# Optimization experiments

Hardware: AMD Instinct MI355X
Metric: run time of the kernel (lower is better)

Reference implementation:

```python
import jax, jax.numpy as jnp
import numpy as np
import math

B, S, HID, H = 2, 2048, 2048, 16
D = HID // H  # head_dim = 128


def rotate_half(x):
    x1, x2 = x[..., : x.shape[-1] // 2], x[..., x.shape[-1] // 2:]
    return jnp.concatenate((-x2, x1), axis=-1)


def setup_inputs() -> dict:
    key = jax.random.key(0)
    ks = jax.random.split(key, 6)
    x = jax.random.normal(ks[0], (B, S, HID), dtype=jnp.float32)
    # learned projection weights (torch Linear: y = x @ W.T); store as [in, out]
    scale = 1.0 / math.sqrt(HID)
    Wq = jax.random.normal(ks[1], (HID, HID), dtype=jnp.float32) * scale
    Wk = jax.random.normal(ks[2], (HID, HID), dtype=jnp.float32) * scale
    Wv = jax.random.normal(ks[3], (HID, HID), dtype=jnp.float32) * scale
    Wo = jax.random.normal(ks[4], (HID, HID), dtype=jnp.float32) * scale
    # causal additive mask [1,1,S,S]
    causal = jnp.tril(jnp.ones((S, S), dtype=bool))
    attention_mask = jnp.where(causal, 0.0, -1e9).astype(jnp.float32)[None, None]
    # ALiBi bias: slope per head times key position, broadcast over queries
    slopes = 2.0 ** (-8.0 * (jnp.arange(1, H + 1, dtype=jnp.float32) / H))
    alibi = (-slopes[:, None] * jnp.arange(S, dtype=jnp.float32)[None, :])[None, :, None, :]  # [1,H,1,S]
    # RoPE tables broadcastable to [B,H,S,D]
    inv_freq = 1.0 / (10000.0 ** (jnp.arange(0, D // 2, dtype=jnp.float32) / (D // 2)))
    t = jnp.arange(S, dtype=jnp.float32)
    freqs = t[:, None] * inv_freq[None, :]            # [S, D/2]
    emb = jnp.concatenate((freqs, freqs), axis=-1)    # [S, D]
    freqs_cos = jnp.cos(emb)[None, None]              # [1,1,S,D]
    freqs_sin = jnp.sin(emb)[None, None]
    return {"x": x, "Wq": Wq, "Wk": Wk, "Wv": Wv, "Wo": Wo,
            "attention_mask": attention_mask, "alibi": alibi,
            "freqs_cos": freqs_cos, "freqs_sin": freqs_sin}


def reference(x, Wq, Wk, Wv, Wo, attention_mask, alibi, freqs_cos, freqs_sin):
    b, s, _ = x.shape
    def split_heads(y):
        return y.reshape(b, s, H, D).transpose(0, 2, 1, 3)  # [B,H,S,D]
    q = split_heads(x @ Wq)
    k = split_heads(x @ Wk)
    v = split_heads(x @ Wv)
    q = q * freqs_cos + rotate_half(q) * freqs_sin
    k = k * freqs_cos + rotate_half(k) * freqs_sin
    scores = jnp.einsum('bhqd,bhkd->bhqk', q, k) / math.sqrt(D)
    scores = scores + attention_mask + alibi
    attn = jax.nn.softmax(scores, axis=-1)  # dropout p=0 (eval) -> identity
    out = jnp.einsum('bhqk,bhkd->bhqd', attn, v)
    out = out.transpose(0, 2, 1, 3).reshape(b, s, HID)
    return out @ Wo
```

## Files before the change

### kernel.cpp

```cpp
#include <hip/hip_runtime.h>

#define S_LEN   2048
#define HEADS   16
#define HID_DIM 2048
#define HEAD_D  128
#define BATCH   2

typedef __bf16          bf16x8 __attribute__((ext_vector_type(8)));
typedef unsigned short  u16x8  __attribute__((ext_vector_type(8)));
typedef unsigned short  u16x4  __attribute__((ext_vector_type(4)));
typedef float           f32x4  __attribute__((ext_vector_type(4)));

__device__ __forceinline__ unsigned short f2bf(float f) {
  unsigned u = __builtin_bit_cast(unsigned, f);
  u += 0x7FFFu + ((u >> 16) & 1u);
  return (unsigned short)(u >> 16);
}
__device__ __forceinline__ float bf2f(unsigned short s) {
  unsigned u = ((unsigned)s) << 16;
  return __builtin_bit_cast(float, u);
}

__device__ __forceinline__ f32x4 mfma16(u16x8 a, u16x8 b, f32x4 c) {
  return __builtin_amdgcn_mfma_f32_16x16x32_bf16(
      __builtin_bit_cast(bf16x8, a), __builtin_bit_cast(bf16x8, b), c, 0, 0, 0);
}

__device__ __forceinline__ void async_load16(const void* g, void* l) {
  __builtin_amdgcn_global_load_lds(
      (const __attribute__((address_space(1))) void*)g,
      (__attribute__((address_space(3))) void*)l, 16, 0, 0);
}

__global__ __launch_bounds__(256) void cvt_bf16(const float* __restrict__ in,
                                                unsigned short* __restrict__ out,
                                                int n8) {
  for (int i = blockIdx.x * blockDim.x + threadIdx.x; i < n8;
       i += gridDim.x * blockDim.x) {
    const float4* p = (const float4*)in + 2L * i;
    float4 a = p[0], b = p[1];
    u16x8 v;
    v[0] = f2bf(a.x); v[1] = f2bf(a.y); v[2] = f2bf(a.z); v[3] = f2bf(a.w);
    v[4] = f2bf(b.x); v[5] = f2bf(b.y); v[6] = f2bf(b.z); v[7] = f2bf(b.w);
    ((u16x8*)out)[i] = v;
  }
}

__global__ __launch_bounds__(256) void transpose_cvt3(
    const float* __restrict__ W0, const float* __restrict__ W1,
    const float* __restrict__ W2, unsigned short* __restrict__ O0,
    unsigned short* __restrict__ O1, unsigned short* __restrict__ O2,
    int dim) {
  __shared__ float tile[32][33];
  const int z = blockIdx.z;
  const float* W = (z == 0) ? W0 : (z == 1) ? W1 : W2;
  unsigned short* Wt = (z == 0) ? O0 : (z == 1) ? O1 : O2;
  const int bx = blockIdx.x * 32, by = blockIdx.y * 32;
  const int tx = threadIdx.x, ty = threadIdx.y;
#pragma unroll
  for (int i = 0; i < 32; i += 8)
    tile[ty + i][tx] = W[(long)(by + ty + i) * dim + bx + tx];
  __syncthreads();
#pragma unroll
  for (int i = 0; i < 32; i += 8)
    Wt[(long)(bx + ty + i) * dim + by + tx] = f2bf(tile[tx][ty + i]);
}

__global__ __launch_bounds__(256) void transpose_cvt(const float* __restrict__ W,
                                                     unsigned short* __restrict__ Wt,
                                                     int dim) {
  __shared__ float tile[32][33];
  const int bx = blockIdx.x * 32, by = blockIdx.y * 32;
  const int tx = threadIdx.x, ty = threadIdx.y;
#pragma unroll
  for (int i = 0; i < 32; i += 8)
    tile[ty + i][tx] = W[(long)(by + ty + i) * dim + bx + tx];
  __syncthreads();
#pragma unroll
  for (int i = 0; i < 32; i += 8)
    Wt[(long)(bx + ty + i) * dim + by + tx] = f2bf(tile[tx][ty + i]);
}

__global__ __launch_bounds__(256) void transpose_v(const unsigned short* __restrict__ V,
                                                   unsigned short* __restrict__ Vt) {
  __shared__ unsigned short tile[32][34];
  const int s0 = blockIdx.x * 32, d0 = blockIdx.y * 32, bh = blockIdx.z;
  const int b = bh >> 4, h = bh & 15;
  const int tx = threadIdx.x, ty = threadIdx.y;
#pragma unroll
  for (int i = 0; i < 32; i += 8)
    tile[ty + i][tx] =
        V[(long)(b * S_LEN + s0 + ty + i) * HID_DIM + h * HEAD_D + d0 + tx];
  __syncthreads();
#pragma unroll
  for (int i = 0; i < 32; i += 8)
    Vt[((long)bh * HEAD_D + d0 + ty + i) * S_LEN + s0 + tx] = tile[tx][ty + i];
}

__global__ __launch_bounds__(256) void rope_qk(unsigned short* __restrict__ Qb,
                                               unsigned short* __restrict__ Kb,
                                               const float* __restrict__ fcos,
                                               const float* __restrict__ fsin) {
  const float SC = 0.08838834764831845f;
  const long i = (long)blockIdx.x * blockDim.x + threadIdx.x;
  const int d = (int)(i & 63);
  const int h = (int)((i >> 6) & (HEADS - 1));
  const long row = i >> 10;
  const int s = (int)(row & (S_LEN - 1));
  const long base = row * HID_DIM + h * HEAD_D + d;
  const float c0 = fcos[s * HEAD_D + d], c1 = fcos[s * HEAD_D + d + 64];
  const float s0 = fsin[s * HEAD_D + d], s1 = fsin[s * HEAD_D + d + 64];
  const float q0 = bf2f(Qb[base]), q1 = bf2f(Qb[base + 64]);
  Qb[base]      = f2bf((q0 * c0 - q1 * s0) * SC);
  Qb[base + 64] = f2bf((q1 * c1 + q0 * s1) * SC);
  const float k0 = bf2f(Kb[base]), k1 = bf2f(Kb[base + 64]);
  Kb[base]      = f2bf(k0 * c0 - k1 * s0);
  Kb[base + 64] = f2bf(k1 * c1 + k0 * s1);
}

__global__ __launch_bounds__(256, 3) void gemm10(
    const unsigned short* __restrict__ A,
    const unsigned short* __restrict__ Bt0,
    unsigned short* __restrict__ Cb0,
    float* __restrict__ Cf,
    int M, int N, int K, long zsB, long zsC) {
  __shared__ __align__(16) unsigned short Abuf[3][128 * 32];
  __shared__ __align__(16) unsigned short Bbuf[3][128 * 32];
  const int t = threadIdx.x;
  const int lane = t & 63;
  const int w = t >> 6;
  const int wr = w >> 1, wc = w & 1;
  const int l15 = lane & 15, l4 = lane >> 4;

  const int nwg = gridDim.x;
  const int bid = blockIdx.x;
  const int sw = (bid & 7) * (nwg >> 3) + (bid >> 3);
  const int nbx = N >> 7, nby = M >> 7;
  const int z = sw / (nbx * nby);
  const int rem = sw - z * nbx * nby;
  const int by = rem / nbx;
  const int bx = rem - by * nbx;

  const unsigned short* Bt = Bt0 + (long)z * zsB;
  unsigned short* Cb = Cb0 ? Cb0 + (long)z * zsC : nullptr;

  f32x4 acc[4][4] = {};

  const int kcol = 8 * ((t & 3) ^ ((t >> 3) & 3));
  const unsigned short* aSrc = A + ((long)by * 128 + (t >> 2)) * K + kcol;
  const unsigned short* bSrc = Bt + ((long)bx * 128 + (t >> 2)) * K + kcol;

  const int swzr = 8 * (l4 ^ ((l15 >> 1) & 3));
  const int aROff = (wr * 64 + l15) * 32 + swzr;
  const int bROff = (wc * 64 + l15) * 32 + swzr;

  const int NT = K >> 5;

#define STG(slot, kt_) do {                                              \
    async_load16(aSrc + (long)(kt_) * 32,                                \
                 (char*)(&Abuf[slot][0]) + t * 16);                      \
    async_load16(aSrc + (long)(kt_) * 32 + 64L * K,                      \
                 (char*)(&Abuf[slot][0]) + 4096 + t * 16);               \
    async_load16(bSrc + (long)(kt_) * 32,                                \
                 (char*)(&Bbuf[slot][0]) + t * 16);                      \
    async_load16(bSrc + (long)(kt_) * 32 + 64L * K,                      \
                 (char*)(&Bbuf[slot][0]) + 4096 + t * 16);               \
  } while (0)

  STG(0, 0);
  STG(1, 1);
  asm volatile("s_waitcnt vmcnt(4)" ::: "memory");
  __builtin_amdgcn_s_barrier();

  int cur = 0;
  for (int kt = 0; kt < NT; ++kt) {
    const unsigned short* Ab = &Abuf[cur][0];
    const unsigned short* Bb = &Bbuf[cur][0];
    const bool stg = (kt + 2) < NT;
    u16x8 af[4], bfr[4];
#pragma unroll
    for (int n = 0; n < 4; ++n) bfr[n] = *(const u16x8*)&Bb[bROff + n * 512];
#pragma unroll
    for (int m = 0; m < 4; ++m) af[m] = *(const u16x8*)&Ab[aROff + m * 512];
    if (stg) {
      const int s2 = (cur + 2 >= 3) ? cur - 1 : cur + 2;
      STG(s2, kt + 2);
    }
    __builtin_amdgcn_s_setprio(1);
#pragma unroll
    for (int m = 0; m < 4; ++m)
#pragma unroll
      for (int n = 0; n < 4; ++n)
        acc[m][n] = mfma16(af[m], bfr[n], acc[m][n]);
    __builtin_amdgcn_s_setprio(0);
    __builtin_amdgcn_sched_barrier(0);
    if (kt + 1 < NT) {
      if (stg) asm volatile("s_waitcnt vmcnt(4)" ::: "memory");
      else     asm volatile("s_waitcnt vmcnt(0)" ::: "memory");
      __builtin_amdgcn_s_barrier();
    }
    cur = (cur + 1 >= 3) ? 0 : cur + 1;
  }
#undef STG

  const long orow = (long)by * 128 + wr * 64 + l4 * 4;
  const long ocol = (long)bx * 128 + wc * 64 + l15;
#pragma unroll
  for (int m = 0; m < 4; ++m)
#pragma unroll
    for (int n = 0; n < 4; ++n)
#pragma unroll
      for (int r = 0; r < 4; ++r) {
        const long row = orow + m * 16 + r;
        const long col = ocol + n * 16;
        if (Cb) Cb[row * N + col] = f2bf(acc[m][n][r]);
        else    Cf[row * N + col] = acc[m][n][r];
      }
}

__global__ __launch_bounds__(256, 4) void attn_fwd7(
    const unsigned short* __restrict__ Q,
    const unsigned short* __restrict__ K,
    const unsigned short* __restrict__ Vt,
    const float* __restrict__ alibi,
    unsigned short* __restrict__ O) {
  __shared__ __align__(16) unsigned short Kl[2][32 * 128];
  __shared__ __align__(16) unsigned short Vl[2][64 * 64];
  __shared__ __align__(16) unsigned short Pl[4][32][40];
  const int t = threadIdx.x;
  const int lane = t & 63;
  const int w = t >> 6;
  const int l15 = lane & 15, l4 = lane >> 4;

  const int bid = blockIdx.x;
  const int xcd = bid & 7;
  const int idx = bid >> 3;
  const int qh = idx >> 4;
  const int ql = idx & 15;
  const int qt = (qh < 2) ? ql : (15 - ql);
  const int bh = xcd * 4 + qh;
  const int b = bh >> 4, h = bh & 15;
  const int q0b = qt * 128;
  const int q0 = q0b + w * 32;
  const float nslope = alibi[h * S_LEN + 1];

  const long rowbase = ((long)b * S_LEN) * HID_DIM + h * HEAD_D;
  const long vtbase  = ((long)bh * HEAD_D) * S_LEN;

  u16x8 qf[2][4];
  {
    const unsigned short* qp = Q + rowbase + (long)(q0 + l15) * HID_DIM + l4 * 8;
#pragma unroll
    for (int m = 0; m < 2; ++m)
#pragma unroll
      for (int ds = 0; ds < 4; ++ds)
        qf[m][ds] = *(const u16x8*)(qp + (long)m * 16 * HID_DIM + ds * 32);
  }

  f32x4 acc[2][8] = {};
  float m_r[2] = {-1e30f, -1e30f};
  float l_r[2] = {0.f, 0.f};

  int dd, rw, cbl;
  dd = 16 * t;        rw = dd >> 8; cbl = (dd & 255) ^ ((rw & 7) << 4);
  const unsigned short* ksrc0 = K + rowbase + (long)rw * HID_DIM + (cbl >> 1);
  dd = 4096 + 16 * t; rw = dd >> 8; cbl = (dd & 255) ^ ((rw & 7) << 4);
  const unsigned short* ksrc1 = K + rowbase + (long)rw * HID_DIM + (cbl >> 1);
  dd = 16 * t;        rw = dd >> 7; cbl = (dd & 127) ^ ((rw & 3) << 4);
  const unsigned short* vsrc0 =
      Vt + vtbase + (long)(2 * rw + (cbl >> 6)) * S_LEN + ((cbl & 63) >> 1);
  dd = 4096 + 16 * t; rw = dd >> 7; cbl = (dd & 127) ^ ((rw & 3) << 4);
  const unsigned short* vsrc1 =
      Vt + vtbase + (long)(2 * rw + (cbl >> 6)) * S_LEN + ((cbl & 63) >> 1);

#define ASTAGE(buf, kt_) do {                                             \
    const long kadd = (long)(kt_) * 32 * HID_DIM;                         \
    async_load16(ksrc0 + kadd, (char*)(&Kl[buf][0]) + 16 * t);            \
    async_load16(ksrc1 + kadd, (char*)(&Kl[buf][0]) + 4096 + 16 * t);     \
    async_load16(vsrc0 + (kt_) * 32, (char*)(&Vl[buf][0]) + 16 * t);      \
    async_load16(vsrc1 + (kt_) * 32, (char*)(&Vl[buf][0]) + 4096 + 16 * t); \
  } while (0)

  const int ntB = qt * 4 + 4;
  const int mykt = q0 >> 5;

  ASTAGE(0, 0);
  __syncthreads();

  int cur = 0;
  for (int kt = 0; kt < ntB; ++kt) {
    const int kb = kt * 32;
    if (kt + 1 < ntB) ASTAGE(cur ^ 1, kt + 1);
    if (kt <= mykt) {
      const char* Kc = (const char*)&Kl[cur][0];
      const char* Vc = (const char*)&Vl[cur][0];
      f32x4 sacc[2][2] = {};
#pragma unroll
      for (int ds = 0; ds < 4; ++ds) {
        u16x8 kfr[2];
#pragma unroll
        for (int n = 0; n < 2; ++n) {
          const int R = 16 * n + l15;
          const int cb = (ds * 64 + l4 * 16) ^ ((l15 & 7) << 4);
          kfr[n] = *(const u16x8*)(Kc + R * 256 + cb);
        }
#pragma unroll
        for (int n = 0; n < 2; ++n)
#pragma unroll
          for (int m = 0; m < 2; ++m)
            sacc[n][m] = mfma16(kfr[n], qf[m][ds], sacc[n][m]);
      }
#pragma unroll
      for (int m = 0; m < 2; ++m) {
        const int q = q0 + 16 * m + l15;
        float pv[2][4];
        float rmax = -1e30f;
#pragma unroll
        for (int n = 0; n < 2; ++n)
#pragma unroll
          for (int r = 0; r < 4; ++r) {
            const int k = kb + 16 * n + l4 * 4 + r;
            float v = sacc[n][m][r] + nslope * (float)k;
            if (k > q) v = -1e30f;
            pv[n][r] = v;
            rmax = fmaxf(rmax, v);
          }
        rmax = fmaxf(rmax, __shfl_xor(rmax, 16, 64));
        rmax = fmaxf(rmax, __shfl_xor(rmax, 32, 64));
        const float mnew = fmaxf(m_r[m], rmax);
        const float sf = __expf(m_r[m] - mnew);
        m_r[m] = mnew;
        float rsum = 0.f;
#pragma unroll
        for (int n = 0; n < 2; ++n)
#pragma unroll
          for (int r = 0; r < 4; ++r) {
            pv[n][r] = __expf(pv[n][r] - mnew);
            rsum += pv[n][r];
          }
        rsum += __shfl_xor(rsum, 16, 64);
        rsum += __shfl_xor(rsum, 32, 64);
        l_r[m] = l_r[m] * sf + rsum;
        float sfo[4];
#pragma unroll
        for (int r = 0; r < 4; ++r) sfo[r] = __shfl(sf, l4 * 4 + r, 64);
#pragma unroll
        for (int dt = 0; dt < 8; ++dt)
#pragma unroll
          for (int r = 0; r < 4; ++r) acc[m][dt][r] *= sfo[r];
#pragma unroll
        for (int n = 0; n < 2; ++n) {
          u16x4 pk;
#pragma unroll
          for (int r = 0; r < 4; ++r) pk[r] = f2bf(pv[n][r]);
          *(u16x4*)&Pl[w][16 * m + l15][16 * n + l4 * 4] = pk;
        }
      }
      u16x8 pf[2];
#pragma unroll
      for (int m = 0; m < 2; ++m)
        pf[m] = *(const u16x8*)&Pl[w][16 * m + l15][l4 * 8];
#pragma unroll
      for (int dt = 0; dt < 8; ++dt) {
        const int d = dt * 16 + l15;
        const int vrow = d >> 1;
        const int cbv = (((d & 1) << 6) | (l4 << 4)) ^ ((vrow & 3) << 4);
        u16x8 vb = *(const u16x8*)(Vc + vrow * 128 + cbv);
#pragma unroll
        for (int m = 0; m < 2; ++m)
          acc[m][dt] = mfma16(pf[m], vb, acc[m][dt]);
      }
    }
    __builtin_amdgcn_sched_barrier(0);
    __syncthreads();
    cur ^= 1;
  }
#undef ASTAGE

#pragma unroll
  for (int m = 0; m < 2; ++m) {
    float linv[4];
#pragma unroll
    for (int r = 0; r < 4; ++r)
      linv[r] = 1.0f / __shfl(l_r[m], l4 * 4 + r, 64);
#pragma unroll
    for (int dt = 0; dt < 8; ++dt)
#pragma unroll
      for (int r = 0; r < 4; ++r) {
        const long row = q0 + 16 * m + l4 * 4 + r;
        O[rowbase + row * HID_DIM + dt * 16 + l15] = f2bf(acc[m][dt][r] * linv[r]);
      }
  }
}

extern "C" void kernel_launch(void* const* d_in, const int* in_sizes, int n_in,
                              void* d_out, int out_size, void* d_ws, size_t ws_size,
                              hipStream_t stream) {
  const float* x    = (const float*)d_in[0];
  const float* Wq   = (const float*)d_in[1];
  const float* Wk   = (const float*)d_in[2];
  const float* Wv   = (const float*)d_in[3];
  const float* Wo   = (const float*)d_in[4];
  const float* alibi = (const float*)d_in[6];
  const float* fcos  = (const float*)d_in[7];
  const float* fsin  = (const float*)d_in[8];

  char* ws = (char*)d_ws;
  unsigned short* xb  = (unsigned short*)(ws);
  unsigned short* wtq = (unsigned short*)(ws + (16L << 20));
  unsigned short* wtk = (unsigned short*)(ws + (24L << 20));
  unsigned short* wtv = (unsigned short*)(ws + (32L << 20));
  unsigned short* VtG = (unsigned short*)(ws + (24L << 20));
  unsigned short* Qb  = (unsigned short*)(ws + (40L << 20));
  unsigned short* Kb  = (unsigned short*)(ws + (56L << 20));
  unsigned short* Vb  = (unsigned short*)(ws + (72L << 20));

  const int M = BATCH * S_LEN;
  const int N = HID_DIM;
  const int K = HID_DIM;

  cvt_bf16<<<2048, 256, 0, stream>>>(x, xb, M * K / 8);

  dim3 tb(32, 8);
  transpose_cvt3<<<dim3(N / 32, K / 32, 3), tb, 0, stream>>>(
      Wq, Wk, Wv, wtq, wtk, wtv, N);

  gemm10<<<3 * (M / 128) * (N / 128), 256, 0, stream>>>(
      xb, wtq, Qb, nullptr, M, N, K,
      (long)HID_DIM * HID_DIM, (long)(8 << 20));

  rope_qk<<<(BATCH * S_LEN * HEADS * 64) / 256, 256, 0, stream>>>(Qb, Kb, fcos, fsin);

  transpose_v<<<dim3(S_LEN / 32, HEAD_D / 32, BATCH * HEADS), tb, 0, stream>>>(Vb, VtG);

  transpose_cvt<<<dim3(N / 32, K / 32), tb, 0, stream>>>(Wo, wtq, N);

  attn_fwd7<<<512, 256, 0, stream>>>(Qb, Kb, VtG, alibi, xb);

  gemm10<<<(M / 128) * (N / 128), 256, 0, stream>>>(
      xb, wtq, nullptr, (float*)d_out, M, N, K, 0L, 0L);
}
```

Baseline: 308.0 us.

## Load GEMM B fragments directly from global memory and defer softmax rescaling

The GEMM is rewritten as a templated kernel with a BMx256 output tile. Each wave owns 64 output columns and reads its B operand fragments straight from global memory instead of staging them in shared memory. Only A is staged through LDS, which cuts LDS traffic and footprint and allows different tile heights for the QKV and output projections. The attention kernel now rescales the running max and accumulator only when a row max grows by more than a threshold, skipping the per-tile exp and accumulator multiply. This trades exact max tracking for the risk of larger exponent values, and the direct global B loads have no latency hiding beyond caching.

```diff
diff --git a/kernel.cpp b/kernel.cpp
--- a/kernel.cpp
+++ b/kernel.cpp
@@ -118,24 +118,25 @@
   Kb[base + 64] = f2bf(k1 * c1 + k0 * s1);
 }
 
-__global__ __launch_bounds__(256, 3) void gemm10(
+template <int BM>
+__global__ __launch_bounds__(256, 2) void gemm11(
     const unsigned short* __restrict__ A,
     const unsigned short* __restrict__ Bt0,
     unsigned short* __restrict__ Cb0,
     float* __restrict__ Cf,
     int M, int N, int K, long zsB, long zsC) {
-  __shared__ __align__(16) unsigned short Abuf[3][128 * 32];
-  __shared__ __align__(16) unsigned short Bbuf[3][128 * 32];
+  constexpr int MF = BM / 16;
+  constexpr int AL = BM / 64;
+  __shared__ __align__(16) unsigned short Abuf[3][BM * 32];
   const int t = threadIdx.x;
   const int lane = t & 63;
   const int w = t >> 6;
-  const int wr = w >> 1, wc = w & 1;
   const int l15 = lane & 15, l4 = lane >> 4;
 
   const int nwg = gridDim.x;
   const int bid = blockIdx.x;
   const int sw = (bid & 7) * (nwg >> 3) + (bid >> 3);
-  const int nbx = N >> 7, nby = M >> 7;
+  const int nbx = N >> 8, nby = M / BM;
   const int z = sw / (nbx * nby);
   const int rem = sw - z * nbx * nby;
   const int by = rem / nbx;
@@ -144,58 +145,54 @@
   const unsigned short* Bt = Bt0 + (long)z * zsB;
   unsigned short* Cb = Cb0 ? Cb0 + (long)z * zsC : nullptr;
 
-  f32x4 acc[4][4] = {};
+  f32x4 acc[MF][4] = {};
 
   const int kcol = 8 * ((t & 3) ^ ((t >> 3) & 3));
-  const unsigned short* aSrc = A + ((long)by * 128 + (t >> 2)) * K + kcol;
-  const unsigned short* bSrc = Bt + ((long)bx * 128 + (t >> 2)) * K + kcol;
+  const unsigned short* aSrc = A + ((long)by * BM + (t >> 2)) * K + kcol;
+  const unsigned short* bP = Bt + ((long)bx * 256 + w * 64 + l15) * K + l4 * 8;
 
   const int swzr = 8 * (l4 ^ ((l15 >> 1) & 3));
-  const int aROff = (wr * 64 + l15) * 32 + swzr;
-  const int bROff = (wc * 64 + l15) * 32 + swzr;
 
   const int NT = K >> 5;
 
 #define STG(slot, kt_) do {                                              \
     async_load16(aSrc + (long)(kt_) * 32,                                \
                  (char*)(&Abuf[slot][0]) + t * 16);                      \
-    async_load16(aSrc + (long)(kt_) * 32 + 64L * K,                      \
-                 (char*)(&Abuf[slot][0]) + 4096 + t * 16);               \
-    async_load16(bSrc + (long)(kt_) * 32,                                \
-                 (char*)(&Bbuf[slot][0]) + t * 16);                      \
-    async_load16(bSrc + (long)(kt_) * 32 + 64L * K,                      \
-                 (char*)(&Bbuf[slot][0]) + 4096 + t * 16);               \
+    if (AL == 2)                                                         \
+      async_load16(aSrc + (long)(kt_) * 32 + 64L * K,                    \
+                   (char*)(&Abuf[slot][0]) + 4096 + t * 16);             \
   } while (0)
 
   STG(0, 0);
   STG(1, 1);
-  asm volatile("s_waitcnt vmcnt(4)" ::: "memory");
+  asm volatile("s_waitcnt vmcnt(%0)" ::"n"(AL) : "memory");
   __builtin_amdgcn_s_barrier();
 
   int cur = 0;
   for (int kt = 0; kt < NT; ++kt) {
-    const unsigned short* Ab = &Abuf[cur][0];
-    const unsigned short* Bb = &Bbuf[cur][0];
     const bool stg = (kt + 2) < NT;
-    u16x8 af[4], bfr[4];
-#pragma unroll
-    for (int n = 0; n < 4; ++n) bfr[n] = *(const u16x8*)&Bb[bROff + n * 512];
-#pragma unroll
-    for (int m = 0; m < 4; ++m) af[m] = *(const u16x8*)&Ab[aROff + m * 512];
+    u16x8 bfr[4];
+#pragma unroll
+    for (int n = 0; n < 4; ++n)
+      bfr[n] = *(const u16x8*)(bP + (long)(16 * n) * K + (long)kt * 32);
+    u16x8 af[MF];
+#pragma unroll
+    for (int m = 0; m < MF; ++m)
+      af[m] = *(const u16x8*)&Abuf[cur][(m * 16 + l15) * 32 + swzr];
     if (stg) {
       const int s2 = (cur + 2 >= 3) ? cur - 1 : cur + 2;
       STG(s2, kt + 2);
     }
     __builtin_amdgcn_s_setprio(1);
 #pragma unroll
-    for (int m = 0; m < 4; ++m)
+    for (int m = 0; m < MF; ++m)
 #pragma unroll
       for (int n = 0; n < 4; ++n)
         acc[m][n] = mfma16(af[m], bfr[n], acc[m][n]);
     __builtin_amdgcn_s_setprio(0);
     __builtin_amdgcn_sched_barrier(0);
     if (kt + 1 < NT) {
-      if (stg) asm volatile("s_waitcnt vmcnt(4)" ::: "memory");
+      if (stg) asm volatile("s_waitcnt vmcnt(%0)" ::"n"(AL) : "memory");
       else     asm volatile("s_waitcnt vmcnt(0)" ::: "memory");
       __builtin_amdgcn_s_barrier();
     }
@@ -203,10 +200,10 @@
   }
 #undef STG
 
-  const long orow = (long)by * 128 + wr * 64 + l4 * 4;
-  const long ocol = (long)bx * 128 + wc * 64 + l15;
-#pragma unroll
-  for (int m = 0; m < 4; ++m)
+  const long orow = (long)by * BM + l4 * 4;
+  const long ocol = (long)bx * 256 + w * 64 + l15;
+#pragma unroll
+  for (int m = 0; m < MF; ++m)
 #pragma unroll
     for (int n = 0; n < 4; ++n)
 #pragma unroll
@@ -218,7 +215,7 @@
       }
 }
 
-__global__ __launch_bounds__(256, 4) void attn_fwd7(
+__global__ __launch_bounds__(256, 4) void attn_fwd8(
     const unsigned short* __restrict__ Q,
     const unsigned short* __restrict__ K,
     const unsigned short* __restrict__ Vt,
@@ -327,27 +324,30 @@
           }
         rmax = fmaxf(rmax, __shfl_xor(rmax, 16, 64));
         rmax = fmaxf(rmax, __shfl_xor(rmax, 32, 64));
-        const float mnew = fmaxf(m_r[m], rmax);
-        const float sf = __expf(m_r[m] - mnew);
-        m_r[m] = mnew;
+        if (__ballot(rmax > m_r[m] + 8.f)) {
+          const float mnew = fmaxf(m_r[m], rmax);
+          const float sf = __expf(m_r[m] - mnew);
+          m_r[m] = mnew;
+          l_r[m] *= sf;
+          float sfo[4];
+#pragma unroll
+          for (int r = 0; r < 4; ++r) sfo[r] = __shfl(sf, l4 * 4 + r, 64);
+#pragma unroll
+          for (int dt = 0; dt < 8; ++dt)
+#pragma unroll
+            for (int r = 0; r < 4; ++r) acc[m][dt][r] *= sfo[r];
+        }
         float rsum = 0.f;
 #pragma unroll
         for (int n = 0; n < 2; ++n)
 #pragma unroll
           for (int r = 0; r < 4; ++r) {
-            pv[n][r] = __expf(pv[n][r] - mnew);
+            pv[n][r] = __expf(pv[n][r] - m_r[m]);
             rsum += pv[n][r];
           }
         rsum += __shfl_xor(rsum, 16, 64);
         rsum += __shfl_xor(rsum, 32, 64);
-        l_r[m] = l_r[m] * sf + rsum;
-        float sfo[4];
-#pragma unroll
-        for (int r = 0; r < 4; ++r) sfo[r] = __shfl(sf, l4 * 4 + r, 64);
-#pragma unroll
-        for (int dt = 0; dt < 8; ++dt)
-#pragma unroll
-          for (int r = 0; r < 4; ++r) acc[m][dt][r] *= sfo[r];
+        l_r[m] += rsum;
 #pragma unroll
         for (int n = 0; n < 2; ++n) {
           u16x4 pk;
@@ -425,7 +425,7 @@
   transpose_cvt3<<<dim3(N / 32, K / 32, 3), tb, 0, stream>>>(
       Wq, Wk, Wv, wtq, wtk, wtv, N);
 
-  gemm10<<<3 * (M / 128) * (N / 128), 256, 0, stream>>>(
+  gemm11<128><<<3 * (M / 128) * (N / 256), 256, 0, stream>>>(
       xb, wtq, Qb, nullptr, M, N, K,
       (long)HID_DIM * HID_DIM, (long)(8 << 20));
 
@@ -435,8 +435,8 @@
 
   transpose_cvt<<<dim3(N / 32, K / 32), tb, 0, stream>>>(Wo, wtq, N);
 
-  attn_fwd7<<<512, 256, 0, stream>>>(Qb, Kb, VtG, alibi, xb);
-
-  gemm10<<<(M / 128) * (N / 128), 256, 0, stream>>>(
+  attn_fwd8<<<512, 256, 0, stream>>>(Qb, Kb, VtG, alibi, xb);
+
+  gemm11<64><<<(M / 64) * (N / 256), 256, 0, stream>>>(
       xb, wtq, nullptr, (float*)d_out, M, N, K, 0L, 0L);
 }
```

Measured after the change: 376.7 us. 22.3% more time.
